# Performance work log

Measured on AMD Instinct MI355X. Metric: run time of the kernel, lower is better.

Reference implementation:

```python
import jax, jax.numpy as jnp
import numpy as np
import math

N_HEAD = 16
N_HEAD_KV = 4
HEAD_DIM = 128
N_EMBD = 2048

def alibi_slopes(n_heads):
    def pow2_slopes(n):
        start = 2 ** (-2 ** (-(math.log2(n) - 3)))
        return [start * start ** i for i in range(n)]
    if math.log2(n_heads).is_integer():
        return jnp.array(pow2_slopes(n_heads), dtype=jnp.float32)
    closest = 2 ** math.floor(math.log2(n_heads))
    base = pow2_slopes(closest)
    if n_heads <= 2 * closest:
        s = base + base[0::2]
    else:
        s = base + base[0::2] + base[1::2]
    return jnp.array(s[:n_heads], dtype=jnp.float32)

def setup_inputs() -> dict:
    key = jax.random.key(0)
    ks = jax.random.split(key, 5)
    B, T, C = 2, 2048, N_EMBD
    kvdim = N_HEAD_KV * HEAD_DIM
    sc = 0.02
    return {
        "x": jax.random.normal(ks[0], (B, T, C), dtype=jnp.float32),
        "q_w": jax.random.normal(ks[1], (C, C), dtype=jnp.float32) * sc,
        "k_w": jax.random.normal(ks[2], (kvdim, C), dtype=jnp.float32) * sc,
        "v_w": jax.random.normal(ks[3], (kvdim, C), dtype=jnp.float32) * sc,
        "o_w": jax.random.normal(ks[4], (C, C), dtype=jnp.float32) * sc,
    }

def reference(x, q_w, k_w, v_w, o_w):
    B, T, C = x.shape
    H, Hkv, D = N_HEAD, N_HEAD_KV, HEAD_DIM
    # nan/inf sanitize (no-op for random inputs, kept for fidelity)
    x = jnp.nan_to_num(x, nan=0.0, posinf=10000.0, neginf=-10000.0)
    q = (x @ q_w.T).reshape(B, T, H, D).transpose(0, 2, 1, 3)      # [B,H,T,D]
    k = (x @ k_w.T).reshape(B, T, Hkv, D).transpose(0, 2, 1, 3)    # [B,Hkv,T,D]
    v = (x @ v_w.T).reshape(B, T, Hkv, D).transpose(0, 2, 1, 3)
    # repeat_interleave KV heads to H heads
    rep = H // Hkv
    k = jnp.repeat(k, rep, axis=1)
    v = jnp.repeat(v, rep, axis=1)
    scale = 1.0 / math.sqrt(D)
    att = jnp.einsum('bhqd,bhkd->bhqk', q, k) * scale
    att = jnp.clip(att, -10000.0, 10000.0)
    pos = jnp.arange(T)
    causal = jnp.where(pos[None, :] > pos[:, None], -jnp.inf, 0.0)  # [T,T]
    slopes = alibi_slopes(H)  # [H]
    rel = (pos[None, :] - pos[:, None]).astype(jnp.float32)         # [T,T]
    alibi = slopes[:, None, None] * rel[None]                        # [H,T,T]
    att = att + causal[None, None] + alibi[None]
    att = jax.nn.softmax(att.astype(jnp.float32), axis=-1).astype(q.dtype)
    y = jnp.einsum('bhqk,bhkd->bhqd', att, v)
    y = jnp.nan_to_num(y, nan=0.0, posinf=10000.0, neginf=-10000.0)
    y = y.transpose(0, 2, 1, 3).reshape(B, T, C)
    return y @ o_w.T
```

## Files before the change

kernel.cpp:

```cpp
#include <hip/hip_runtime.h>
#include <hip/hip_bf16.h>
#include <math.h>

#define SEQ   2048
#define EMBD  2048
#define NH    16
#define NKV   4
#define HD    128
#define NQKV  3072
#define NUNITS 512

typedef __attribute__((ext_vector_type(8))) short short8;
typedef __attribute__((ext_vector_type(4))) short short4v;
typedef __attribute__((ext_vector_type(4))) float floatx4;

static __device__ __forceinline__ short f2bf(float f) {
    union { float f; unsigned u; } cv; cv.f = f;
    unsigned u = cv.u;
    u += 0x7FFF + ((u >> 16) & 1);
    return (short)(u >> 16);
}

#define GL16(gsrc, ldst)                                                        \
    __builtin_amdgcn_global_load_lds(                                           \
        (const __attribute__((address_space(1))) void*)(gsrc),                  \
        (__attribute__((address_space(3))) void*)(ldst), 16, 0, 0)

static __device__ __forceinline__ int alibi_window(float slope2) {
    return (int)ceilf((42.0f / slope2 + 63.0f) * (1.0f / 64.0f));
}

static __device__ __forceinline__ int unit_cost(int h, int p) {
    float slope2 = exp2f(-0.5f * (float)(h + 1)) * 1.44269504f;
    int W = alibi_window(slope2);
    return min(W + 1, 2 * p + 2);
}

__global__ void cvt_all(const float* __restrict__ x,  const float* __restrict__ qw,
                        const float* __restrict__ kw, const float* __restrict__ vw,
                        const float* __restrict__ ow,
                        short* __restrict__ xb, short* __restrict__ wall,
                        short* __restrict__ owb) {
    int i = blockIdx.x * blockDim.x + threadIdx.x;
    const float* src; short* dst; int off;
    if (i < 2097152)      { src = x;  dst = xb;             off = i; }
    else if (i < 3145728) { src = qw; dst = wall;           off = i - 2097152; }
    else if (i < 3407872) { src = kw; dst = wall + 4194304; off = i - 3145728; }
    else if (i < 3670016) { src = vw; dst = wall + 5242880; off = i - 3407872; }
    else                  { src = ow; dst = owb;            off = i - 3670016; }
    float4 v = ((const float4*)src)[off];
    float a[4] = {v.x, v.y, v.z, v.w};
    short4v o;
#pragma unroll
    for (int j = 0; j < 4; ++j) {
        float f = a[j];
        f = isnan(f) ? 0.0f : fminf(fmaxf(f, -10000.0f), 10000.0f);
        o[j] = f2bf(f);
    }
    ((short4v*)dst)[off] = o;
}

__global__ void attn_setup(int* __restrict__ qtab) {
    __shared__ int keys[NUNITS];
    int i = threadIdx.x;
    int hp = i >> 1;
    int key = unit_cost(hp >> 4, hp & 15) * 1024 + i;
    keys[i] = key;
    __syncthreads();
    int rank = 0;
    for (int j = 0; j < NUNITS; ++j) rank += (keys[j] > key);
    qtab[rank] = i;
}

template<int MODE>
__global__ __launch_bounds__(256) void gemm_bt(
    const short* __restrict__ A, const short* __restrict__ W,
    float* __restrict__ Cout, int M, int N, int K,
    short* __restrict__ qb, short* __restrict__ kb, short* __restrict__ vb)
{
    __shared__ __align__(16) short sA[128 * 64];
    __shared__ __align__(16) short sB[128 * 64];

    const int tid  = threadIdx.x;
    const int lane = tid & 63;
    const int wv   = tid >> 6;
    const int wr   = wv >> 1, wc = wv & 1;
    const int lr   = lane & 15, lg = lane >> 4;
    const int bn   = blockIdx.x, bm = blockIdx.y;

    const short* gA[4]; const short* gB[4];
    short* lA[4]; short* lB[4];
#pragma unroll
    for (int s = 0; s < 4; ++s) {
        int ck  = wv * 256 + s * 64 + lane;
        int row = ck >> 3, seg = ck & 7;
        int segSw = seg ^ (row & 7);
        gA[s] = A + (size_t)(bm * 128 + row) * K + segSw * 8;
        gB[s] = W + (size_t)(bn * 128 + row) * K + segSw * 8;
        lA[s] = &sA[(wv * 256 + s * 64) * 8];
        lB[s] = &sB[(wv * 256 + s * 64) * 8];
    }

    floatx4 acc[4][4] = {};
    const int nkt = K / 64;
    for (int kt = 0; kt < nkt; ++kt) {
#pragma unroll
        for (int s = 0; s < 4; ++s) {
            GL16(gA[s] + kt * 64, lA[s]);
            GL16(gB[s] + kt * 64, lB[s]);
        }
        __syncthreads();

#pragma unroll
        for (int ks = 0; ks < 2; ++ks) {
            short8 af[4], bfr[4];
#pragma unroll
            for (int i = 0; i < 4; ++i) {
                int ra = wr * 64 + i * 16 + lr;
                int rb = wc * 64 + i * 16 + lr;
                af[i]  = *(const short8*)&sA[ra * 64 + (((ks * 4 + lg) ^ (ra & 7)) * 8)];
                bfr[i] = *(const short8*)&sB[rb * 64 + (((ks * 4 + lg) ^ (rb & 7)) * 8)];
            }
#pragma unroll
            for (int i = 0; i < 4; ++i)
#pragma unroll
                for (int j = 0; j < 4; ++j)
                    acc[i][j] = __builtin_amdgcn_mfma_f32_16x16x32_bf16(af[i], bfr[j], acc[i][j], 0, 0, 0);
        }
        __syncthreads();
    }

    const float QSCALE = 0.08838834764831845f * 1.44269504f;
#pragma unroll
    for (int i = 0; i < 4; ++i)
#pragma unroll
        for (int j = 0; j < 4; ++j)
#pragma unroll
            for (int r = 0; r < 4; ++r) {
                int gm = bm * 128 + wr * 64 + i * 16 + lg * 4 + r;
                int gn = bn * 128 + wc * 64 + j * 16 + lr;
                float v = acc[i][j][r];
                if (MODE == 0) {
                    int b = gm >> 11, t = gm & (SEQ - 1);
                    if (gn < 2048) {
                        int h = gn >> 7, d = gn & 127;
                        qb[(((size_t)(b * NH + h)) * SEQ + t) * HD + d] = f2bf(v * QSCALE);
                    } else if (gn < 2560) {
                        int hk = (gn - 2048) >> 7, d = gn & 127;
                        kb[(((size_t)(b * NKV + hk)) * SEQ + t) * HD + d] = f2bf(v);
                    } else {
                        int hv = (gn - 2560) >> 7, d = gn & 127;
                        vb[(((size_t)(b * NKV + hv)) * HD + d) * SEQ + t] = f2bf(v);
                    }
                } else {
                    Cout[(size_t)gm * N + gn] = v;
                }
            }
}

__global__ __launch_bounds__(512, 4) void attn_fwd(
    const short* __restrict__ Q, const short* __restrict__ Kg,
    const short* __restrict__ VT, short* __restrict__ Y,
    const int* __restrict__ qtab)
{
    __shared__ __align__(16) short sK[2][64 * 128];
    __shared__ __align__(16) short sV[128 * 64];
    __shared__ short Plds[8][16][72];

    const int tid  = threadIdx.x;
    const int wave = tid >> 6, lane = tid & 63;
    const int lr = lane & 15, lg = lane >> 4;
    const int bid = blockIdx.x;

    const int rank = (bid < 256) ? bid : (767 - bid);
    const int uu = qtab[rank];
    const int b = uu & 1, hp = uu >> 1;
    const int h = hp >> 4, p = hp & 15;
    const int hkv = h >> 2;
    const int qgw = 2 * p + (wave < 4 ? 1 : 0);

    const short* Qb = Q  +  ((size_t)(b * NH  + h  )) * SEQ * HD;
    const short* Kp = Kg +  ((size_t)(b * NKV + hkv)) * SEQ * HD;
    const short* Vp = VT +  ((size_t)(b * NKV + hkv)) * HD * SEQ;

    const float slope2 = exp2f(-0.5f * (float)(h + 1)) * 1.44269504f;
    const int W = alibi_window(slope2);
    const int thi = 2 * p + 1;
    int tlo = thi - W; if (tlo < 0) tlo = 0;

    const short* gK[2]; const short* gV[2];
    int lOff[2];
#pragma unroll
    for (int j = 0; j < 2; ++j) {
        int ck = wave * 128 + j * 64 + lane;
        int krow = ck >> 4, kseg = ck & 15;
        gK[j] = Kp + (size_t)krow * HD + (kseg ^ (krow & 7)) * 8;
        int vrow = ck >> 3, vseg = ck & 7;
        gV[j] = Vp + (size_t)vrow * SEQ + (vseg ^ (vrow & 7)) * 8;
        lOff[j] = (wave * 128 + j * 64) * 8;
    }

    float c_nt[4];
#pragma unroll
    for (int nt = 0; nt < 4; ++nt) c_nt[nt] = slope2 * (float)(nt * 16 + lr);

    const int q0 = qgw * 64 + (wave & 3) * 16;
    short8 qf[4];
#pragma unroll
    for (int cc = 0; cc < 4; ++cc)
        qf[cc] = *(const short8*)&Qb[(size_t)(q0 + lr) * HD + cc * 32 + lg * 8];

    floatx4 po[8] = {};
    float m[4], lsum[4];
#pragma unroll
    for (int r = 0; r < 4; ++r) { m[r] = -3.0e38f; lsum[r] = 0.0f; }

    int cur = 0;
#pragma unroll
    for (int j = 0; j < 2; ++j)
        GL16(gK[j] + (size_t)(thi << 6) * HD, &sK[0][0] + lOff[j]);
    __syncthreads();

#pragma unroll 1
    for (int t = thi; t >= tlo; --t) {
#pragma unroll
        for (int j = 0; j < 2; ++j)
            GL16(gV[j] + (t << 6), &sV[0] + lOff[j]);
        if (t > tlo) {
#pragma unroll
            for (int j = 0; j < 2; ++j)
                GL16(gK[j] + (size_t)((t - 1) << 6) * HD, &sK[cur ^ 1][0] + lOff[j]);
        }

        const bool active = (t <= qgw) && (t > qgw - W);
        const int kv0 = t << 6;

        if (active) {
            const short* kr = &sK[cur][0];
            floatx4 sf[4];
#pragma unroll
            for (int nt = 0; nt < 4; ++nt) {
                floatx4 sacc = {0.f, 0.f, 0.f, 0.f};
#pragma unroll
                for (int cc = 0; cc < 4; ++cc) {
                    int krow = nt * 16 + lr;
                    short8 kf = *(const short8*)&kr[krow * 128 + (((cc * 4 + lg) ^ (krow & 7)) * 8)];
                    sacc = __builtin_amdgcn_mfma_f32_16x16x32_bf16(qf[cc], kf, sacc, 0, 0, 0);
                }
                sf[nt] = sacc;
            }

            const float a2t = slope2 * (float)kv0;
            const bool masked = (t == qgw);
#pragma unroll
            for (int r = 0; r < 4; ++r) {
                const int qpos = q0 + lg * 4 + r;
                float sv[4];
#pragma unroll
                for (int nt = 0; nt < 4; ++nt)
                    sv[nt] = sf[nt][r] + a2t + c_nt[nt];
                if (masked) {
#pragma unroll
                    for (int nt = 0; nt < 4; ++nt) {
                        int kpos = kv0 + nt * 16 + lr;
                        if (kpos > qpos) sv[nt] = -3.0e38f;
                    }
                }
                bool over = (sv[0] > m[r]) | (sv[1] > m[r]) | (sv[2] > m[r]) | (sv[3] > m[r]);
                if (__any(over)) {
                    float mx = fmaxf(fmaxf(sv[0], sv[1]), fmaxf(sv[2], sv[3]));
#pragma unroll
                    for (int off = 1; off < 16; off <<= 1) mx = fmaxf(mx, __shfl_xor(mx, off));
                    float mn = fmaxf(m[r], mx);
                    float rs = exp2f(m[r] - mn);
                    lsum[r] *= rs;
#pragma unroll
                    for (int dt = 0; dt < 8; ++dt) po[dt][r] *= rs;
                    m[r] = mn;
                }
#pragma unroll
                for (int nt = 0; nt < 4; ++nt) {
                    float pp = exp2f(sv[nt] - m[r]);
                    lsum[r] += pp;
                    Plds[wave][lg * 4 + r][nt * 16 + lr] = f2bf(pp);
                }
            }
        }

        __syncthreads();

        if (active) {
            short8 pf0 = *(const short8*)&Plds[wave][lr][lg * 8];
            short8 pf1 = *(const short8*)&Plds[wave][lr][32 + lg * 8];
#pragma unroll
            for (int dt = 0; dt < 8; ++dt) {
                int vrow = dt * 16 + lr;
                short8 vf0 = *(const short8*)&sV[vrow * 64 + (((lg    ) ^ (vrow & 7)) * 8)];
                short8 vf1 = *(const short8*)&sV[vrow * 64 + (((lg + 4) ^ (vrow & 7)) * 8)];
                po[dt] = __builtin_amdgcn_mfma_f32_16x16x32_bf16(pf0, vf0, po[dt], 0, 0, 0);
                po[dt] = __builtin_amdgcn_mfma_f32_16x16x32_bf16(pf1, vf1, po[dt], 0, 0, 0);
            }
        }

        __syncthreads();
        cur ^= 1;
    }

#pragma unroll
    for (int r = 0; r < 4; ++r) {
        float sum = lsum[r];
#pragma unroll
        for (int off = 1; off < 16; off <<= 1) sum += __shfl_xor(sum, off);
        float inv = 1.0f / sum;
        int row = q0 + lg * 4 + r;
#pragma unroll
        for (int dt = 0; dt < 8; ++dt)
            Y[((size_t)(b * SEQ + row)) * EMBD + h * HD + dt * 16 + lr] = f2bf(po[dt][r] * inv);
    }
}

extern "C" void kernel_launch(void* const* d_in, const int* in_sizes, int n_in,
                              void* d_out, int out_size, void* d_ws, size_t ws_size,
                              hipStream_t stream) {
    const float* x   = (const float*)d_in[0];
    const float* q_w = (const float*)d_in[1];
    const float* k_w = (const float*)d_in[2];
    const float* v_w = (const float*)d_in[3];
    const float* o_w = (const float*)d_in[4];
    float* out = (float*)d_out;

    char* ws = (char*)d_ws;
    short* x_bf  = (short*)(ws);
    short* w_all = (short*)(ws + 16777216);
    short* o_wb  = (short*)(ws + 29360128);
    short* q_b   = (short*)(ws + 37748736);
    short* k_b   = (short*)(ws + 54525952);
    short* vT_b  = (short*)(ws + 58720256);
    short* y_b   = (short*)(ws + 62914560);
    int*   qtab  = (int*)(ws);

    cvt_all<<<18432, 256, 0, stream>>>(x, q_w, k_w, v_w, o_w, x_bf, w_all, o_wb);

    gemm_bt<0><<<dim3(NQKV / 128, 4096 / 128), 256, 0, stream>>>(
        x_bf, w_all, nullptr, 4096, NQKV, EMBD, q_b, k_b, vT_b);

    attn_setup<<<1, NUNITS, 0, stream>>>(qtab);
    attn_fwd<<<512, 512, 0, stream>>>(q_b, k_b, vT_b, y_b, qtab);

    gemm_bt<1><<<dim3(EMBD / 128, 4096 / 128), 256, 0, stream>>>(
        y_b, o_wb, out, 4096, EMBD, EMBD, nullptr, nullptr, nullptr);
}
```

Before: 212.4 us.

## Process two query tiles per wave in attention to reuse K/V fragments

```diff
diff --git a/kernel.cpp b/kernel.cpp
--- a/kernel.cpp
+++ b/kernel.cpp
@@ -158,14 +158,14 @@
             }
 }
 
-__global__ __launch_bounds__(512, 4) void attn_fwd(
+__global__ __launch_bounds__(256) void attn_fwd(
     const short* __restrict__ Q, const short* __restrict__ Kg,
     const short* __restrict__ VT, short* __restrict__ Y,
     const int* __restrict__ qtab)
 {
     __shared__ __align__(16) short sK[2][64 * 128];
     __shared__ __align__(16) short sV[128 * 64];
-    __shared__ short Plds[8][16][72];
+    __shared__ short Plds[4][2][16][72];
 
     const int tid  = threadIdx.x;
     const int wave = tid >> 6, lane = tid & 63;
@@ -177,7 +177,7 @@
     const int b = uu & 1, hp = uu >> 1;
     const int h = hp >> 4, p = hp & 15;
     const int hkv = h >> 2;
-    const int qgw = 2 * p + (wave < 4 ? 1 : 0);
+    const int qgA = 2 * p + 1, qgB = 2 * p;
 
     const short* Qb = Q  +  ((size_t)(b * NH  + h  )) * SEQ * HD;
     const short* Kp = Kg +  ((size_t)(b * NKV + hkv)) * SEQ * HD;
@@ -185,120 +185,166 @@
 
     const float slope2 = exp2f(-0.5f * (float)(h + 1)) * 1.44269504f;
     const int W = alibi_window(slope2);
-    const int thi = 2 * p + 1;
+    const int thi = qgA;
     int tlo = thi - W; if (tlo < 0) tlo = 0;
 
-    const short* gK[2]; const short* gV[2];
-    int lOff[2];
-#pragma unroll
-    for (int j = 0; j < 2; ++j) {
-        int ck = wave * 128 + j * 64 + lane;
+    const short* gK[4]; const short* gV[4];
+    int lOff[4];
+#pragma unroll
+    for (int j = 0; j < 4; ++j) {
+        int ck = wave * 256 + j * 64 + lane;
         int krow = ck >> 4, kseg = ck & 15;
         gK[j] = Kp + (size_t)krow * HD + (kseg ^ (krow & 7)) * 8;
         int vrow = ck >> 3, vseg = ck & 7;
         gV[j] = Vp + (size_t)vrow * SEQ + (vseg ^ (vrow & 7)) * 8;
-        lOff[j] = (wave * 128 + j * 64) * 8;
+        lOff[j] = (wave * 256 + j * 64) * 8;
     }
 
     float c_nt[4];
 #pragma unroll
     for (int nt = 0; nt < 4; ++nt) c_nt[nt] = slope2 * (float)(nt * 16 + lr);
 
-    const int q0 = qgw * 64 + (wave & 3) * 16;
-    short8 qf[4];
-#pragma unroll
-    for (int cc = 0; cc < 4; ++cc)
-        qf[cc] = *(const short8*)&Qb[(size_t)(q0 + lr) * HD + cc * 32 + lg * 8];
-
-    floatx4 po[8] = {};
-    float m[4], lsum[4];
-#pragma unroll
-    for (int r = 0; r < 4; ++r) { m[r] = -3.0e38f; lsum[r] = 0.0f; }
+    const int q0A = qgA * 64 + wave * 16;
+    const int q0B = qgB * 64 + wave * 16;
+    short8 qfA[4], qfB[4];
+#pragma unroll
+    for (int cc = 0; cc < 4; ++cc) {
+        qfA[cc] = *(const short8*)&Qb[(size_t)(q0A + lr) * HD + cc * 32 + lg * 8];
+        qfB[cc] = *(const short8*)&Qb[(size_t)(q0B + lr) * HD + cc * 32 + lg * 8];
+    }
+
+    floatx4 poA[8] = {}, poB[8] = {};
+    float mA[4], lsA[4], mB[4], lsB[4];
+#pragma unroll
+    for (int r = 0; r < 4; ++r) { mA[r] = mB[r] = -3.0e38f; lsA[r] = lsB[r] = 0.0f; }
 
     int cur = 0;
 #pragma unroll
-    for (int j = 0; j < 2; ++j)
+    for (int j = 0; j < 4; ++j)
         GL16(gK[j] + (size_t)(thi << 6) * HD, &sK[0][0] + lOff[j]);
     __syncthreads();
 
 #pragma unroll 1
     for (int t = thi; t >= tlo; --t) {
 #pragma unroll
-        for (int j = 0; j < 2; ++j)
+        for (int j = 0; j < 4; ++j)
             GL16(gV[j] + (t << 6), &sV[0] + lOff[j]);
         if (t > tlo) {
 #pragma unroll
-            for (int j = 0; j < 2; ++j)
+            for (int j = 0; j < 4; ++j)
                 GL16(gK[j] + (size_t)((t - 1) << 6) * HD, &sK[cur ^ 1][0] + lOff[j]);
         }
 
-        const bool active = (t <= qgw) && (t > qgw - W);
+        const bool activeB = (t <= qgB) && (t > qgB - W);
         const int kv0 = t << 6;
 
-        if (active) {
-            const short* kr = &sK[cur][0];
-            floatx4 sf[4];
-#pragma unroll
-            for (int nt = 0; nt < 4; ++nt) {
-                floatx4 sacc = {0.f, 0.f, 0.f, 0.f};
-#pragma unroll
-                for (int cc = 0; cc < 4; ++cc) {
-                    int krow = nt * 16 + lr;
-                    short8 kf = *(const short8*)&kr[krow * 128 + (((cc * 4 + lg) ^ (krow & 7)) * 8)];
-                    sacc = __builtin_amdgcn_mfma_f32_16x16x32_bf16(qf[cc], kf, sacc, 0, 0, 0);
-                }
-                sf[nt] = sacc;
-            }
-
-            const float a2t = slope2 * (float)kv0;
-            const bool masked = (t == qgw);
+        const short* kr = &sK[cur][0];
+        floatx4 sfA[4], sfB[4];
+#pragma unroll
+        for (int nt = 0; nt < 4; ++nt) {
+            floatx4 sa = {0.f, 0.f, 0.f, 0.f};
+            floatx4 sb = {0.f, 0.f, 0.f, 0.f};
+#pragma unroll
+            for (int cc = 0; cc < 4; ++cc) {
+                int krow = nt * 16 + lr;
+                short8 kf = *(const short8*)&kr[krow * 128 + (((cc * 4 + lg) ^ (krow & 7)) * 8)];
+                sa = __builtin_amdgcn_mfma_f32_16x16x32_bf16(qfA[cc], kf, sa, 0, 0, 0);
+                sb = __builtin_amdgcn_mfma_f32_16x16x32_bf16(qfB[cc], kf, sb, 0, 0, 0);
+            }
+            sfA[nt] = sa; sfB[nt] = sb;
+        }
+
+        const float a2t = slope2 * (float)kv0;
+        {
+            const bool masked = (t == thi);
 #pragma unroll
             for (int r = 0; r < 4; ++r) {
-                const int qpos = q0 + lg * 4 + r;
+                const int qpos = q0A + lg * 4 + r;
                 float sv[4];
 #pragma unroll
                 for (int nt = 0; nt < 4; ++nt)
-                    sv[nt] = sf[nt][r] + a2t + c_nt[nt];
+                    sv[nt] = sfA[nt][r] + a2t + c_nt[nt];
                 if (masked) {
 #pragma unroll
-                    for (int nt = 0; nt < 4; ++nt) {
-                        int kpos = kv0 + nt * 16 + lr;
-                        if (kpos > qpos) sv[nt] = -3.0e38f;
-                    }
-                }
-                bool over = (sv[0] > m[r]) | (sv[1] > m[r]) | (sv[2] > m[r]) | (sv[3] > m[r]);
+                    for (int nt = 0; nt < 4; ++nt)
+                        if (kv0 + nt * 16 + lr > qpos) sv[nt] = -3.0e38f;
+                }
+                bool over = (sv[0] > mA[r]) | (sv[1] > mA[r]) | (sv[2] > mA[r]) | (sv[3] > mA[r]);
                 if (__any(over)) {
                     float mx = fmaxf(fmaxf(sv[0], sv[1]), fmaxf(sv[2], sv[3]));
 #pragma unroll
                     for (int off = 1; off < 16; off <<= 1) mx = fmaxf(mx, __shfl_xor(mx, off));
-                    float mn = fmaxf(m[r], mx);
-                    float rs = exp2f(m[r] - mn);
-                    lsum[r] *= rs;
-#pragma unroll
-                    for (int dt = 0; dt < 8; ++dt) po[dt][r] *= rs;
-                    m[r] = mn;
+                    float mn = fmaxf(mA[r], mx);
+                    float rs = exp2f(mA[r] - mn);
+                    lsA[r] *= rs;
+#pragma unroll
+                    for (int dt = 0; dt < 8; ++dt) poA[dt][r] *= rs;
+                    mA[r] = mn;
                 }
 #pragma unroll
                 for (int nt = 0; nt < 4; ++nt) {
-                    float pp = exp2f(sv[nt] - m[r]);
-                    lsum[r] += pp;
-                    Plds[wave][lg * 4 + r][nt * 16 + lr] = f2bf(pp);
+                    float pp = exp2f(sv[nt] - mA[r]);
+                    lsA[r] += pp;
+                    Plds[wave][0][lg * 4 + r][nt * 16 + lr] = f2bf(pp);
+                }
+            }
+        }
+        if (activeB) {
+            const bool masked = (t == qgB);
+#pragma unroll
+            for (int r = 0; r < 4; ++r) {
+                const int qpos = q0B + lg * 4 + r;
+                float sv[4];
+#pragma unroll
+                for (int nt = 0; nt < 4; ++nt)
+                    sv[nt] = sfB[nt][r] + a2t + c_nt[nt];
+                if (masked) {
+#pragma unroll
+                    for (int nt = 0; nt < 4; ++nt)
+                        if (kv0 + nt * 16 + lr > qpos) sv[nt] = -3.0e38f;
+                }
+                bool over = (sv[0] > mB[r]) | (sv[1] > mB[r]) | (sv[2] > mB[r]) | (sv[3] > mB[r]);
+                if (__any(over)) {
+                    float mx = fmaxf(fmaxf(sv[0], sv[1]), fmaxf(sv[2], sv[3]));
+#pragma unroll
+                    for (int off = 1; off < 16; off <<= 1) mx = fmaxf(mx, __shfl_xor(mx, off));
+                    float mn = fmaxf(mB[r], mx);
+                    float rs = exp2f(mB[r] - mn);
+                    lsB[r] *= rs;
+#pragma unroll
+                    for (int dt = 0; dt < 8; ++dt) poB[dt][r] *= rs;
+                    mB[r] = mn;
+                }
+#pragma unroll
+                for (int nt = 0; nt < 4; ++nt) {
+                    float pp = exp2f(sv[nt] - mB[r]);
+                    lsB[r] += pp;
+                    Plds[wave][1][lg * 4 + r][nt * 16 + lr] = f2bf(pp);
                 }
             }
         }
 
         __syncthreads();
 
-        if (active) {
-            short8 pf0 = *(const short8*)&Plds[wave][lr][lg * 8];
-            short8 pf1 = *(const short8*)&Plds[wave][lr][32 + lg * 8];
+        {
+            short8 pA0 = *(const short8*)&Plds[wave][0][lr][lg * 8];
+            short8 pA1 = *(const short8*)&Plds[wave][0][lr][32 + lg * 8];
+            short8 pB0, pB1;
+            if (activeB) {
+                pB0 = *(const short8*)&Plds[wave][1][lr][lg * 8];
+                pB1 = *(const short8*)&Plds[wave][1][lr][32 + lg * 8];
+            }
 #pragma unroll
             for (int dt = 0; dt < 8; ++dt) {
                 int vrow = dt * 16 + lr;
                 short8 vf0 = *(const short8*)&sV[vrow * 64 + (((lg    ) ^ (vrow & 7)) * 8)];
                 short8 vf1 = *(const short8*)&sV[vrow * 64 + (((lg + 4) ^ (vrow & 7)) * 8)];
-                po[dt] = __builtin_amdgcn_mfma_f32_16x16x32_bf16(pf0, vf0, po[dt], 0, 0, 0);
-                po[dt] = __builtin_amdgcn_mfma_f32_16x16x32_bf16(pf1, vf1, po[dt], 0, 0, 0);
+                poA[dt] = __builtin_amdgcn_mfma_f32_16x16x32_bf16(pA0, vf0, poA[dt], 0, 0, 0);
+                poA[dt] = __builtin_amdgcn_mfma_f32_16x16x32_bf16(pA1, vf1, poA[dt], 0, 0, 0);
+                if (activeB) {
+                    poB[dt] = __builtin_amdgcn_mfma_f32_16x16x32_bf16(pB0, vf0, poB[dt], 0, 0, 0);
+                    poB[dt] = __builtin_amdgcn_mfma_f32_16x16x32_bf16(pB1, vf1, poB[dt], 0, 0, 0);
+                }
             }
         }
 
@@ -308,14 +354,19 @@
 
 #pragma unroll
     for (int r = 0; r < 4; ++r) {
-        float sum = lsum[r];
-#pragma unroll
-        for (int off = 1; off < 16; off <<= 1) sum += __shfl_xor(sum, off);
-        float inv = 1.0f / sum;
-        int row = q0 + lg * 4 + r;
-#pragma unroll
-        for (int dt = 0; dt < 8; ++dt)
-            Y[((size_t)(b * SEQ + row)) * EMBD + h * HD + dt * 16 + lr] = f2bf(po[dt][r] * inv);
+        float sA = lsA[r], sB = lsB[r];
+#pragma unroll
+        for (int off = 1; off < 16; off <<= 1) {
+            sA += __shfl_xor(sA, off);
+            sB += __shfl_xor(sB, off);
+        }
+        float invA = 1.0f / sA, invB = 1.0f / sB;
+        int rowA = q0A + lg * 4 + r, rowB = q0B + lg * 4 + r;
+#pragma unroll
+        for (int dt = 0; dt < 8; ++dt) {
+            Y[((size_t)(b * SEQ + rowA)) * EMBD + h * HD + dt * 16 + lr] = f2bf(poA[dt][r] * invA);
+            Y[((size_t)(b * SEQ + rowB)) * EMBD + h * HD + dt * 16 + lr] = f2bf(poB[dt][r] * invB);
+        }
     }
 }
 
@@ -345,7 +396,7 @@
         x_bf, w_all, nullptr, 4096, NQKV, EMBD, q_b, k_b, vT_b);
 
     attn_setup<<<1, NUNITS, 0, stream>>>(qtab);
-    attn_fwd<<<512, 512, 0, stream>>>(q_b, k_b, vT_b, y_b, qtab);
+    attn_fwd<<<512, 256, 0, stream>>>(q_b, k_b, vT_b, y_b, qtab);
 
     gemm_bt<1><<<dim3(EMBD / 128, 4096 / 128), 256, 0, stream>>>(
         y_b, o_wb, out, 4096, EMBD, EMBD, nullptr, nullptr, nullptr);
```

New measurement: 248.3 us. +16.9%, slower.
